# Kernel tuning notes

Hardware: AMD Instinct MI355X
Metric: run time of the kernel (lower is better)

The kernel has to match this reference:

```python
import jax, jax.numpy as jnp
import numpy as np

B, C, H, W = 16, 256, 32, 32
EPS = 1e-6


def setup_inputs() -> dict:
    key = jax.random.key(0)
    ks = jax.random.split(key, 6)
    s = 1.0 / np.sqrt(C)  # conv-like init scale
    return {
        "x": jax.random.normal(ks[0], (B, C, H, W), dtype=jnp.float32),
        "ln_w": jnp.ones((C,), dtype=jnp.float32),
        "ln_b": jnp.zeros((C,), dtype=jnp.float32),
        "wq": jax.random.normal(ks[1], (C, C), dtype=jnp.float32) * s,
        "bq": jnp.zeros((C,), dtype=jnp.float32),
        "wk": jax.random.normal(ks[2], (C, C), dtype=jnp.float32) * s,
        "bk": jnp.zeros((C,), dtype=jnp.float32),
        "wv": jax.random.normal(ks[3], (C, C), dtype=jnp.float32) * s,
        "bv": jnp.zeros((C,), dtype=jnp.float32),
        "wp": jax.random.normal(ks[4], (C, C), dtype=jnp.float32) * s,
        "bp": jnp.zeros((C,), dtype=jnp.float32),
    }


def reference(x, ln_w, ln_b, wq, bq, wk, bk, wv, bv, wp, bp):
    b, c, h, w = x.shape
    n = h * w
    # LayerNorm2d: normalize over channel dim (biased variance)
    mean = jnp.mean(x, axis=1, keepdims=True)
    var = jnp.var(x, axis=1, keepdims=True)
    hn = (x - mean) / jnp.sqrt(var + EPS)
    hn = hn * ln_w[None, :, None, None] + ln_b[None, :, None, None]
    hn = hn.reshape(b, c, n)  # [B, C, N]
    # 1x1 convs == channel matmuls; tokens layout [B, N, C]
    q = jnp.einsum('oc,bcn->bno', wq, hn) + bq  # [B, N, C]
    k = jnp.einsum('oc,bcn->bon', wk, hn) + bk[None, :, None]  # [B, C, N]
    v = jnp.einsum('oc,bcn->bno', wv, hn) + bv  # [B, N, C]
    scale = c ** (-0.5)
    attn = jnp.einsum('bnc,bcm->bnm', q, k) * scale  # [B, N, N]
    attn = jax.nn.softmax(attn, axis=-1)
    # dropout is identity in eval mode (deterministic reference)
    out = jnp.einsum('bnm,bmc->bnc', attn, v)  # [B, N, C]
    out = jnp.einsum('oc,bnc->bon', wp, out) + bp[None, :, None]  # [B, C, N]
    out = out.reshape(b, c, h, w)
    return x + out
```

## Files before the change

kernel.cpp:

```cpp
#include <hip/hip_runtime.h>
#include <hip/hip_bf16.h>
#include <stdint.h>

typedef __attribute__((ext_vector_type(8))) short bf8_t;
typedef __attribute__((ext_vector_type(4))) float f4_t;
typedef __attribute__((ext_vector_type(16))) float f16x_t;
typedef unsigned short u16;

#define GLOAD16(g, l) __builtin_amdgcn_global_load_lds(                                  \
    (const __attribute__((address_space(1))) void*)(g),                                  \
    (__attribute__((address_space(3))) void*)(l), 16, 0, 0)

__device__ __forceinline__ u16 f2bf(float f) {
    union { float f; unsigned u; } c; c.f = f;
    unsigned u = c.u;
    return (u16)((u + 0x7fffu + ((u >> 16) & 1u)) >> 16);
}

__device__ __forceinline__ unsigned cvt_pk_bf16(float lo, float hi_) {
    unsigned r;
    asm("v_cvt_pk_bf16_f32 %0, %1, %2" : "=v"(r) : "v"(lo), "v"(hi_));
    return r;
}

__global__ void prep_kernel(const float* __restrict__ wq, const float* __restrict__ wk,
                            const float* __restrict__ wv, const float* __restrict__ wp,
                            const float* __restrict__ bq, const float* __restrict__ bk,
                            const float* __restrict__ bv,
                            u16* __restrict__ wcatT, u16* __restrict__ wpt,
                            float* __restrict__ biasc) {
    int idx = blockIdx.x * 256 + threadIdx.x;
    if (idx < 196608) {
        int o = idx >> 8, c = idx & 255;
        float v = (o < 256) ? wq[o * 256 + c]
                : (o < 512) ? wk[(o - 256) * 256 + c]
                            : wv[(o - 512) * 256 + c];
        wcatT[(((c >> 3) * 768) + o) * 8 + (c & 7)] = f2bf(v);
    } else if (idx < 262144) {
        int i = idx - 196608;
        int o = i >> 8, d = i & 255;
        wpt[(((d >> 3) * 256) + o) * 8 + (d & 7)] = f2bf(wp[i]);
    } else if (idx < 262912) {
        int i = idx - 262144;
        biasc[i] = (i < 256) ? bq[i] : (i < 512) ? bk[i - 256] : bv[i - 512];
    }
}

__global__ __launch_bounds__(256) void lnqkv_kernel(
    const float* __restrict__ x, const float* __restrict__ lw,
    const float* __restrict__ lb,
    const u16* __restrict__ wcatT, const float* __restrict__ biasc,
    u16* __restrict__ qbuf, u16* __restrict__ ktp, u16* __restrict__ vtp) {
    __shared__ u16 hn_lds[32 * 64 * 8];
    __shared__ u16 B_lds[2][32 * 64 * 8];
    __shared__ float2 red[4][64];

    const int tid = threadIdx.x;
    const int bid = blockIdx.x;
    const int b = bid >> 4, n0 = (bid & 15) * 64;
    const int tok = tid & 63, cpart = tid >> 6;

    const float* xb = x + (size_t)b * 262144 + n0 + tok;
    float v[64];
    float s = 0.f, s2 = 0.f;
    #pragma unroll
    for (int i = 0; i < 64; i++) {
        v[i] = xb[(size_t)(cpart * 64 + i) * 1024];
        s += v[i]; s2 += v[i] * v[i];
    }
    red[cpart][tok] = make_float2(s, s2);
    __syncthreads();
    s = 0.f; s2 = 0.f;
    #pragma unroll
    for (int gi = 0; gi < 4; gi++) { float2 p = red[gi][tok]; s += p.x; s2 += p.y; }
    float mean = s * 0.00390625f;
    float rstd = rsqrtf(s2 * 0.00390625f - mean * mean + 1e-6f);
    #pragma unroll
    for (int j = 0; j < 8; j++) {
        bf8_t pk;
        #pragma unroll
        for (int e = 0; e < 8; e++) {
            int c = cpart * 64 + j * 8 + e;
            pk[e] = (short)f2bf((v[j * 8 + e] - mean) * rstd * lw[c] + lb[c]);
        }
        *(bf8_t*)&hn_lds[((cpart * 8 + j) * 64 + tok) * 8] = pk;
    }

    const int lane = tid & 63, wv_ = tid >> 6;
    const int lm = lane & 15, lg = lane >> 4;
    const int tw = wv_ & 1, ow = wv_ >> 1;

#define STAGEB(P, BUF)                                                        \
    {                                                                         \
        _Pragma("unroll")                                                     \
        for (int it = 0; it < 8; it++) {                                      \
            int cid = it * 256 + tid;                                         \
            int chunk = cid >> 6, row = cid & 63;                             \
            const u16* gsrc = wcatT + ((size_t)(chunk * 768) + (P) * 64 + row) * 8; \
            GLOAD16(gsrc, &B_lds[BUF][cid * 8]);                              \
        }                                                                     \
    }

    STAGEB(0, 0);
    __syncthreads();

    #pragma unroll
    for (int p = 0; p < 12; p++) {
        const int buf = p & 1;
        if (p < 11) STAGEB(p + 1, buf ^ 1);

        f4_t acc[2][2];
        #pragma unroll
        for (int i = 0; i < 2; i++)
            #pragma unroll
            for (int j = 0; j < 2; j++) acc[i][j] = (f4_t)0.0f;
        #pragma unroll
        for (int kk = 0; kk < 8; kk++) {
            bf8_t af[2], bfr[2];
            #pragma unroll
            for (int i = 0; i < 2; i++)
                af[i] = *(const bf8_t*)&hn_lds[((kk * 4 + lg) * 64 + tw * 32 + i * 16 + lm) * 8];
            #pragma unroll
            for (int j = 0; j < 2; j++)
                bfr[j] = *(const bf8_t*)&B_lds[buf][((kk * 4 + lg) * 64 + ow * 32 + j * 16 + lm) * 8];
            #pragma unroll
            for (int i = 0; i < 2; i++)
                #pragma unroll
                for (int j = 0; j < 2; j++)
                    acc[i][j] = __builtin_amdgcn_mfma_f32_16x16x32_bf16(af[i], bfr[j], acc[i][j], 0, 0, 0);
        }

        #pragma unroll
        for (int i = 0; i < 2; i++)
            #pragma unroll
            for (int j = 0; j < 2; j++)
                #pragma unroll
                for (int r = 0; r < 4; r++) {
                    int loc = tw * 32 + i * 16 + lg * 4 + r;
                    int col = p * 64 + ow * 32 + j * 16 + lm;
                    float val = acc[i][j][r] + biasc[col];
                    int n = n0 + loc;
                    if (col < 256) {
                        qbuf[((size_t)b * 1024 + n) * 256 + col] = f2bf(val * 0.0625f);
                    } else if (col < 512) {
                        int c = col - 256;
                        ktp[(((size_t)b * 32 + (c >> 3)) * 1024 + n) * 8 + (c & 7)] = f2bf(val);
                    } else {
                        int d = col - 512;
                        vtp[(((size_t)b * 128 + (n >> 3)) * 256 + d) * 8 + (n & 7)] = f2bf(val);
                    }
                }
        __syncthreads();
    }
#undef STAGEB
}

__global__ __launch_bounds__(512)
__attribute__((amdgpu_waves_per_eu(2, 2)))
void flash_kernel(const u16* __restrict__ qbuf,
                  const u16* __restrict__ kt,
                  const u16* __restrict__ vt3,
                  const u16* __restrict__ wpt,
                  const float* __restrict__ bp,
                  const float* __restrict__ x,
                  float* __restrict__ out) {
    __shared__ u16 K_lds[2][2][32 * 32 * 8];
    __shared__ u16 V_lds[2][2][4 * 256 * 8];
    __shared__ float lstat[2][32];

    const int flat = blockIdx.x;
    const int xcd = flat & 7, idx = flat >> 3;
    const int b = (xcd << 1) | (idx & 1);
    const int qb = idx >> 1;
    const int tid = threadIdx.x;
    const int wv = tid >> 6, lane = tid & 63;
    const int hi = lane >> 5, lq = lane & 31;
    const int qw = wv & 1, dw = (wv >> 1) & 1, g = wv >> 2;

    const int qrow = qb * 64 + qw * 32 + lq;
    const u16* qptr = qbuf + (size_t)(b * 1024 + qrow) * 256 + hi * 8;
    bf8_t qf[16];
    #pragma unroll
    for (int tc = 0; tc < 16; tc++) qf[tc] = *(const bf8_t*)(qptr + tc * 16);

    float l_r = 0.f;
    f16x_t o_acc[4];
    #pragma unroll
    for (int dt = 0; dt < 4; dt++) o_acc[dt] = (f16x_t)0.0f;

#define STAGE(T, BUF)                                                                     \
    {                                                                                     \
        _Pragma("unroll")                                                                 \
        for (int g2 = 0; g2 < 2; g2++) {                                                  \
            _Pragma("unroll")                                                             \
            for (int it = 0; it < 2; it++) {                                              \
                int cid = it * 512 + tid;                                                 \
                int chunk = cid >> 5, kvl = cid & 31;                                     \
                const u16* gk = kt + (((size_t)b * 32 + chunk) * 1024                     \
                                      + g2 * 512 + (T) * 32 + kvl) * 8;                   \
                GLOAD16(gk, &K_lds[g2][BUF][cid * 8]);                                    \
            }                                                                             \
            _Pragma("unroll")                                                             \
            for (int it = 0; it < 2; it++) {                                              \
                int cid = it * 512 + tid;                                                 \
                int kc = cid >> 8, d = cid & 255;                                         \
                const u16* gv = vt3 + (((size_t)b * 128 + g2 * 64 + (T) * 4 + kc) * 256   \
                                       + d) * 8;                                          \
                GLOAD16(gv, &V_lds[g2][BUF][cid * 8]);                                    \
            }                                                                             \
        }                                                                                 \
    }

    STAGE(0, 0);
    STAGE(1, 1);
    asm volatile("s_waitcnt vmcnt(8)" ::: "memory");
    __builtin_amdgcn_s_barrier();

    for (int t = 0; t < 16; ++t) {
        const int buf = t & 1;

        const u16* kb = &K_lds[g][buf][0];
        bf8_t kf[16];
        #pragma unroll
        for (int tc = 0; tc < 16; tc++)
            kf[tc] = *(const bf8_t*)(kb + ((tc * 2 + hi) * 32 + lq) * 8);

        f16x_t s0 = (f16x_t)0.0f, s1 = (f16x_t)0.0f;
        __builtin_amdgcn_s_setprio(1);
        #pragma unroll
        for (int tc = 0; tc < 8; tc++) {
            s0 = __builtin_amdgcn_mfma_f32_32x32x16_bf16(kf[2 * tc],     qf[2 * tc],     s0, 0, 0, 0);
            s1 = __builtin_amdgcn_mfma_f32_32x32x16_bf16(kf[2 * tc + 1], qf[2 * tc + 1], s1, 0, 0, 0);
        }
        __builtin_amdgcn_s_setprio(0);

        const u16* vb = &V_lds[g][buf][0];
        bf8_t vf[8];
        #pragma unroll
        for (int dt = 0; dt < 4; dt++) {
            int vrow = dw * 128 + dt * 32 + lq;
            vf[2 * dt]     = *(const bf8_t*)(vb + (hi * 256 + vrow) * 8);
            vf[2 * dt + 1] = *(const bf8_t*)(vb + ((2 + hi) * 256 + vrow) * 8);
        }

        f16x_t s = s0 + s1;

        float sum = 0.f;
        #pragma unroll
        for (int r = 0; r < 16; r++) { s[r] = __expf(s[r]); sum += s[r]; }
        l_r += sum;

        unsigned pw[8];
        #pragma unroll
        for (int j = 0; j < 8; j++) pw[j] = cvt_pk_bf16(s[2 * j], s[2 * j + 1]);
        unsigned px[8];
        #pragma unroll
        for (int j = 0; j < 8; j++) px[j] = __shfl_xor((int)pw[j], 32);
        union { unsigned w[4]; bf8_t v; } f0, f1;
        if (hi == 0) {
            f0.w[0] = pw[0]; f0.w[1] = pw[1]; f0.w[2] = px[0]; f0.w[3] = px[1];
            f1.w[0] = pw[4]; f1.w[1] = pw[5]; f1.w[2] = px[4]; f1.w[3] = px[5];
        } else {
            f0.w[0] = px[2]; f0.w[1] = px[3]; f0.w[2] = pw[2]; f0.w[3] = pw[3];
            f1.w[0] = px[6]; f1.w[1] = px[7]; f1.w[2] = pw[6]; f1.w[3] = pw[7];
        }

        asm volatile("s_waitcnt lgkmcnt(0)" ::: "memory");
        __builtin_amdgcn_s_barrier();
        if (t < 14) STAGE(t + 2, buf);

        __builtin_amdgcn_s_setprio(1);
        #pragma unroll
        for (int dt = 0; dt < 4; dt++) {
            o_acc[dt] = __builtin_amdgcn_mfma_f32_32x32x16_bf16(vf[2 * dt],     f0.v, o_acc[dt], 0, 0, 0);
            o_acc[dt] = __builtin_amdgcn_mfma_f32_32x32x16_bf16(vf[2 * dt + 1], f1.v, o_acc[dt], 0, 0, 0);
        }
        __builtin_amdgcn_s_setprio(0);

        if (t < 15) {
            if (t < 14) { asm volatile("s_waitcnt vmcnt(8)" ::: "memory"); }
            else        { asm volatile("s_waitcnt vmcnt(0)" ::: "memory"); }
            __builtin_amdgcn_s_barrier();
        }
    }

    __syncthreads();

    float l_tot = l_r + __shfl_xor(l_r, 32);
    float* obuf = (float*)&K_lds[0][0][0];
    float* rb = obuf + (qw * 2 + dw) * 4096;
    if (g == 1) {
        #pragma unroll
        for (int dt = 0; dt < 4; dt++)
            #pragma unroll
            for (int r = 0; r < 16; r++) {
                int drow = dt * 32 + (r & 3) + 8 * (r >> 2) + 4 * hi;
                rb[drow * 32 + lq] = o_acc[dt][r];
            }
        if (dw == 0 && hi == 0) lstat[qw][lq] = l_tot;
    }
    __syncthreads();

    bf8_t wpf[16];
    #pragma unroll
    for (int tc = 0; tc < 16; tc++)
        wpf[tc] = *(const bf8_t*)(wpt + (((tc * 2 + hi) * 256) + wv * 32 + lq) * 8);

    u16* O16 = (u16*)&V_lds[0][0][0];
    if (g == 0) {
        float inv = 1.0f / (l_tot + lstat[qw][lq]);
        #pragma unroll
        for (int dt = 0; dt < 4; dt++)
            #pragma unroll
            for (int r = 0; r < 16; r++) {
                int drow = dt * 32 + (r & 3) + 8 * (r >> 2) + 4 * hi;
                int d = dw * 128 + drow;
                float val = (o_acc[dt][r] + rb[drow * 32 + lq]) * inv;
                O16[((d >> 3) * 64 + qw * 32 + lq) * 8 + (d & 7)] = f2bf(val);
            }
    }
    __syncthreads();

    f16x_t p0 = (f16x_t)0.0f, p1 = (f16x_t)0.0f;
    __builtin_amdgcn_s_setprio(1);
    #pragma unroll
    for (int tc = 0; tc < 16; tc++) {
        bf8_t of0 = *(const bf8_t*)(O16 + ((tc * 2 + hi) * 64 + lq) * 8);
        bf8_t of1 = *(const bf8_t*)(O16 + ((tc * 2 + hi) * 64 + 32 + lq) * 8);
        p0 = __builtin_amdgcn_mfma_f32_32x32x16_bf16(wpf[tc], of0, p0, 0, 0, 0);
        p1 = __builtin_amdgcn_mfma_f32_32x32x16_bf16(wpf[tc], of1, p1, 0, 0, 0);
    }
    __builtin_amdgcn_s_setprio(0);
    #pragma unroll
    for (int r = 0; r < 16; r++) {
        int crow = wv * 32 + (r & 3) + 8 * (r >> 2) + 4 * hi;
        size_t base = ((size_t)b * 256 + crow) * 1024 + qb * 64;
        float bpv = bp[crow];
        out[base + lq]      = p0[r] + bpv + x[base + lq];
        out[base + 32 + lq] = p1[r] + bpv + x[base + 32 + lq];
    }
#undef STAGE
}

extern "C" void kernel_launch(void* const* d_in, const int* in_sizes, int n_in,
                              void* d_out, int out_size, void* d_ws, size_t ws_size,
                              hipStream_t stream) {
    (void)in_sizes; (void)n_in; (void)out_size; (void)ws_size;
    const float* x   = (const float*)d_in[0];
    const float* lnw = (const float*)d_in[1];
    const float* lnb = (const float*)d_in[2];
    const float* wq  = (const float*)d_in[3];
    const float* bq  = (const float*)d_in[4];
    const float* wk  = (const float*)d_in[5];
    const float* bk  = (const float*)d_in[6];
    const float* wv  = (const float*)d_in[7];
    const float* bv  = (const float*)d_in[8];
    const float* wp  = (const float*)d_in[9];
    const float* bp  = (const float*)d_in[10];
    float* out = (float*)d_out;

    char* ws = (char*)d_ws;
    u16*   wcatT = (u16*)(ws);
    u16*   wpt   = (u16*)(ws + 0x60000);
    float* biasc = (float*)(ws + 0x80000);
    u16*   qbuf  = (u16*)(ws + 0x90000);
    u16*   kt    = (u16*)(ws + 0x890000);
    u16*   vt3   = (u16*)(ws + 0x1090000);

    prep_kernel<<<1028, 256, 0, stream>>>(wq, wk, wv, wp, bq, bk, bv, wcatT, wpt, biasc);
    lnqkv_kernel<<<256, 256, 0, stream>>>(x, lnw, lnb, wcatT, biasc, qbuf, kt, vt3);
    flash_kernel<<<256, 512, 0, stream>>>(qbuf, kt, vt3, wpt, bp, x, out);
}
```

Baseline: 77.18 us.

## Halve LN+QKV token tile and read weights directly from global memory

The LN+QKV kernel now processes 32 tokens per block instead of 64, doubling the grid to 512 blocks for better CU occupancy. The double-buffered LDS staging of the weight matrix is removed: each wave owns 192 output columns and loads B fragments straight from global memory, which drops the per-panel barriers. In exchange, weight reuse across token tiles now depends on L2/L1 caching rather than LDS, and total weight traffic doubles because there are twice as many blocks.

```diff
diff --git a/kernel.cpp b/kernel.cpp
--- a/kernel.cpp
+++ b/kernel.cpp
@@ -51,95 +51,80 @@
     const float* __restrict__ lb,
     const u16* __restrict__ wcatT, const float* __restrict__ biasc,
     u16* __restrict__ qbuf, u16* __restrict__ ktp, u16* __restrict__ vtp) {
-    __shared__ u16 hn_lds[32 * 64 * 8];
-    __shared__ u16 B_lds[2][32 * 64 * 8];
-    __shared__ float2 red[4][64];
+    __shared__ u16 hn_lds[32 * 32 * 8];
+    __shared__ float2 red[8][32];
 
     const int tid = threadIdx.x;
     const int bid = blockIdx.x;
-    const int b = bid >> 4, n0 = (bid & 15) * 64;
-    const int tok = tid & 63, cpart = tid >> 6;
+    const int b = bid >> 5, n0 = (bid & 31) * 32;
+    const int tok = tid & 31, cpart = tid >> 5;
 
     const float* xb = x + (size_t)b * 262144 + n0 + tok;
-    float v[64];
+    float v[32];
     float s = 0.f, s2 = 0.f;
     #pragma unroll
-    for (int i = 0; i < 64; i++) {
-        v[i] = xb[(size_t)(cpart * 64 + i) * 1024];
+    for (int i = 0; i < 32; i++) {
+        v[i] = xb[(size_t)(cpart * 32 + i) * 1024];
         s += v[i]; s2 += v[i] * v[i];
     }
     red[cpart][tok] = make_float2(s, s2);
     __syncthreads();
     s = 0.f; s2 = 0.f;
     #pragma unroll
-    for (int gi = 0; gi < 4; gi++) { float2 p = red[gi][tok]; s += p.x; s2 += p.y; }
+    for (int gi = 0; gi < 8; gi++) { float2 p = red[gi][tok]; s += p.x; s2 += p.y; }
     float mean = s * 0.00390625f;
     float rstd = rsqrtf(s2 * 0.00390625f - mean * mean + 1e-6f);
     #pragma unroll
-    for (int j = 0; j < 8; j++) {
+    for (int j = 0; j < 4; j++) {
         bf8_t pk;
         #pragma unroll
         for (int e = 0; e < 8; e++) {
-            int c = cpart * 64 + j * 8 + e;
+            int c = cpart * 32 + j * 8 + e;
             pk[e] = (short)f2bf((v[j * 8 + e] - mean) * rstd * lw[c] + lb[c]);
         }
-        *(bf8_t*)&hn_lds[((cpart * 8 + j) * 64 + tok) * 8] = pk;
-    }
+        *(bf8_t*)&hn_lds[((cpart * 4 + j) * 32 + tok) * 8] = pk;
+    }
+    __syncthreads();
 
     const int lane = tid & 63, wv_ = tid >> 6;
     const int lm = lane & 15, lg = lane >> 4;
-    const int tw = wv_ & 1, ow = wv_ >> 1;
-
-#define STAGEB(P, BUF)                                                        \
-    {                                                                         \
-        _Pragma("unroll")                                                     \
-        for (int it = 0; it < 8; it++) {                                      \
-            int cid = it * 256 + tid;                                         \
-            int chunk = cid >> 6, row = cid & 63;                             \
-            const u16* gsrc = wcatT + ((size_t)(chunk * 768) + (P) * 64 + row) * 8; \
-            GLOAD16(gsrc, &B_lds[BUF][cid * 8]);                              \
-        }                                                                     \
-    }
-
-    STAGEB(0, 0);
-    __syncthreads();
-
-    #pragma unroll
-    for (int p = 0; p < 12; p++) {
-        const int buf = p & 1;
-        if (p < 11) STAGEB(p + 1, buf ^ 1);
-
-        f4_t acc[2][2];
+    const int colw = wv_ * 192;
+
+    #pragma unroll
+    for (int ct = 0; ct < 3; ct++) {
+        const int cb = colw + ct * 64;
+        f4_t acc[2][4];
         #pragma unroll
         for (int i = 0; i < 2; i++)
             #pragma unroll
-            for (int j = 0; j < 2; j++) acc[i][j] = (f4_t)0.0f;
+            for (int j = 0; j < 4; j++) acc[i][j] = (f4_t)0.0f;
+
         #pragma unroll
         for (int kk = 0; kk < 8; kk++) {
-            bf8_t af[2], bfr[2];
+            bf8_t af[2], bfr[4];
             #pragma unroll
             for (int i = 0; i < 2; i++)
-                af[i] = *(const bf8_t*)&hn_lds[((kk * 4 + lg) * 64 + tw * 32 + i * 16 + lm) * 8];
-            #pragma unroll
-            for (int j = 0; j < 2; j++)
-                bfr[j] = *(const bf8_t*)&B_lds[buf][((kk * 4 + lg) * 64 + ow * 32 + j * 16 + lm) * 8];
+                af[i] = *(const bf8_t*)&hn_lds[((kk * 4 + lg) * 32 + i * 16 + lm) * 8];
+            #pragma unroll
+            for (int j = 0; j < 4; j++)
+                bfr[j] = *(const bf8_t*)(wcatT + (((size_t)(kk * 4 + lg) * 768)
+                                                 + cb + j * 16 + lm) * 8);
             #pragma unroll
             for (int i = 0; i < 2; i++)
                 #pragma unroll
-                for (int j = 0; j < 2; j++)
+                for (int j = 0; j < 4; j++)
                     acc[i][j] = __builtin_amdgcn_mfma_f32_16x16x32_bf16(af[i], bfr[j], acc[i][j], 0, 0, 0);
         }
 
         #pragma unroll
         for (int i = 0; i < 2; i++)
             #pragma unroll
-            for (int j = 0; j < 2; j++)
+            for (int j = 0; j < 4; j++)
                 #pragma unroll
                 for (int r = 0; r < 4; r++) {
-                    int loc = tw * 32 + i * 16 + lg * 4 + r;
-                    int col = p * 64 + ow * 32 + j * 16 + lm;
+                    int n = n0 + i * 16 + lg * 4 + r;
+                    int col = cb + j * 16 + lm;
                     float val = acc[i][j][r] + biasc[col];
-                    int n = n0 + loc;
                     if (col < 256) {
                         qbuf[((size_t)b * 1024 + n) * 256 + col] = f2bf(val * 0.0625f);
                     } else if (col < 512) {
@@ -150,9 +135,7 @@
                         vtp[(((size_t)b * 128 + (n >> 3)) * 256 + d) * 8 + (n & 7)] = f2bf(val);
                     }
                 }
-        __syncthreads();
-    }
-#undef STAGEB
+    }
 }
 
 __global__ __launch_bounds__(512)
@@ -368,6 +351,6 @@
     u16*   vt3   = (u16*)(ws + 0x1090000);
 
     prep_kernel<<<1028, 256, 0, stream>>>(wq, wk, wv, wp, bq, bk, bv, wcatT, wpt, biasc);
-    lnqkv_kernel<<<256, 256, 0, stream>>>(x, lnw, lnb, wcatT, biasc, qbuf, kt, vt3);
+    lnqkv_kernel<<<512, 256, 0, stream>>>(x, lnw, lnb, wcatT, biasc, qbuf, kt, vt3);
     flash_kernel<<<256, 512, 0, stream>>>(qbuf, kt, vt3, wpt, bp, x, out);
 }
```

New measurement: 73.79 us. 1.05x faster.
